# Optimization experiments

Hardware: AMD Instinct MI355X
Metric: run time of the kernel (lower is better)

The kernel has to match this reference:

```python
import jax, jax.numpy as jnp
import numpy as np

N = 50000          # nodes
E = 1_600_000      # directed edges (avg degree 32)
C_IN = 512
C_OUT = 64
H1, F1 = 8, 8      # conv1: heads=8, out per head=8
H2 = 1             # conv2: heads_2=1, concat=False
NEG_SLOPE = 0.2    # GATConv default leaky_relu slope
ELU_ALPHA = 0.2    # F.elu(..., alpha=0.2) in forward


def _glorot(key, shape):
    fan_in, fan_out = shape[0], shape[-1]
    lim = jnp.sqrt(6.0 / (fan_in + fan_out))
    return jax.random.uniform(key, shape, jnp.float32, -lim, lim)


def setup_inputs() -> dict:
    key = jax.random.key(0)
    ks = jax.random.split(key, 12)
    x = jax.random.normal(ks[0], (N, C_IN), jnp.float32)
    edge_index = jax.random.randint(ks[1], (2, E), 0, N, jnp.int32)
    # conv1 params
    W1 = _glorot(ks[2], (C_IN, H1 * F1))
    att_src1 = _glorot(ks[3], (H1, F1))
    att_dst1 = _glorot(ks[4], (H1, F1))
    b1 = jnp.zeros((H1 * F1,), jnp.float32)
    # conv2 params (concat=False, heads=1)
    W2 = _glorot(ks[5], (H1 * F1, H2 * C_OUT))
    att_src2 = _glorot(ks[6], (H2, C_OUT))
    att_dst2 = _glorot(ks[7], (H2, C_OUT))
    b2 = jnp.zeros((C_OUT,), jnp.float32)
    return dict(x=x, edge_index=edge_index, W1=W1, att_src1=att_src1,
                att_dst1=att_dst1, b1=b1, W2=W2, att_src2=att_src2,
                att_dst2=att_dst2, b2=b2)


def gat_conv(x, src, dst, W, att_src, att_dst, bias, concat):
    """PyG GATConv (self-loops already appended to src/dst). Eval mode (no dropout)."""
    n = x.shape[0]
    H, F = att_src.shape
    h = (x @ W).reshape(n, H, F)                       # [N,H,F]
    a_src = jnp.sum(h * att_src, axis=-1)              # [N,H]
    a_dst = jnp.sum(h * att_dst, axis=-1)              # [N,H]
    e = jax.nn.leaky_relu(a_src[src] + a_dst[dst], NEG_SLOPE)  # [E',H]
    # segment softmax over incoming edges of each destination node
    m = jax.ops.segment_max(e, dst, num_segments=n)    # [N,H]
    m = jnp.where(jnp.isfinite(m), m, 0.0)
    ex = jnp.exp(e - m[dst])
    denom = jax.ops.segment_sum(ex, dst, num_segments=n)
    alpha = ex / (denom[dst] + 1e-16)                  # [E',H]
    msg = h[src] * alpha[:, :, None]                   # [E',H,F]
    out = jax.ops.segment_sum(msg, dst, num_segments=n)  # [N,H,F]
    out = out.reshape(n, H * F) if concat else out.mean(axis=1)
    return out + bias


def reference(x, edge_index, W1, att_src1, att_dst1, b1,
              W2, att_src2, att_dst2, b2):
    # add self loops once (GATConv default add_self_loops=True)
    loop = jnp.arange(N, dtype=edge_index.dtype)
    src = jnp.concatenate([edge_index[0], loop])
    dst = jnp.concatenate([edge_index[1], loop])
    # dropout layers are identity in eval mode
    h = gat_conv(x, src, dst, W1, att_src1, att_dst1, b1, concat=True)
    h = jax.nn.elu(h, alpha=ELU_ALPHA)
    out = gat_conv(h, src, dst, W2, att_src2, att_dst2, b2, concat=False)
    return out
```

## Files before the change

### kernel.cpp

```cpp
#include <hip/hip_runtime.h>
#include <hip/hip_bf16.h>
#include <hip/hip_fp16.h>

constexpr int NN   = 50000;
constexpr int NE   = 1600000;
constexpr int CIN  = 512;
constexpr int DH   = 64;
constexpr int H1N  = 8;

constexpr int NB     = 98;
constexpr int TILE   = 8192;
constexpr int NTILES = (NE + TILE - 1) / TILE;
constexpr int BCAP   = 20480;

typedef __attribute__((ext_vector_type(8))) short bf16x8v;
typedef __attribute__((ext_vector_type(4))) float f32x4v;

__device__ __forceinline__ float bf(unsigned short u) {
    union { unsigned int i; float f; } v; v.i = ((unsigned int)u) << 16; return v.f;
}
__device__ __forceinline__ float lrelu(float x) { return fmaxf(x, 0.2f * x); }
__device__ __forceinline__ float ldf(const unsigned short* p, size_t i, bool f32) {
    return f32 ? ((const float*)p)[i] : bf(p[i]);
}
__device__ __forceinline__ unsigned short f2bf(float f) {
    union { float f; unsigned int u; } v; v.f = f;
    unsigned int r = (v.u + 0x7fff + ((v.u >> 16) & 1)) >> 16;
    return (unsigned short)r;
}

__global__ __launch_bounds__(256) void gat_detect(const unsigned short* __restrict__ W1,
                                                  int* __restrict__ flag) {
    __shared__ int cnt;
    if (threadIdx.x == 0) cnt = 0;
    __syncthreads();
    int local = 0;
    for (int i = threadIdx.x; i < 4096; i += 256) {
        unsigned short u = W1[i];
        int e = (u >> 7) & 0xFF;
        if (e >= 140) local++;
    }
    atomicAdd(&cnt, local);
    __syncthreads();
    if (threadIdx.x == 0) flag[0] = (cnt > 100) ? 1 : 0;
}


__global__ __launch_bounds__(256) void gat_bucketA(const int* __restrict__ src,
                                                   const int* __restrict__ dst,
                                                   int* __restrict__ gcnt,
                                                   unsigned int* __restrict__ bucketed) {
    __shared__ int hist[NB];
    __shared__ int cur[NB];
    int t = threadIdx.x;
    if (t < NB) hist[t] = 0;
    __syncthreads();
    int base = blockIdx.x * TILE;
    for (int i = t; i < TILE; i += 256) {
        int e = base + i;
        if (e < NE) atomicAdd(&hist[dst[e] >> 9], 1);
    }
    __syncthreads();
    if (t < NB) cur[t] = hist[t] ? atomicAdd(&gcnt[t], hist[t]) : 0;
    __syncthreads();
    for (int i = t; i < TILE; i += 256) {
        int e = base + i;
        if (e < NE) {
            int d = dst[e];
            int b = d >> 9;
            int p = atomicAdd(&cur[b], 1);
            if (p < BCAP)
                bucketed[(size_t)b * BCAP + p] =
                    ((unsigned int)(d & 511) << 16) | (unsigned int)src[e];
        }
    }
}

__global__ __launch_bounds__(128) void gat_bucketscan(const int* __restrict__ gcnt,
                                                      int* __restrict__ boff,
                                                      int* __restrict__ row_ptr) {
    __shared__ int s[128];
    int t = threadIdx.x;
    s[t] = (t < NB) ? gcnt[t] : 0;
    __syncthreads();
    for (int off = 1; off < 128; off <<= 1) {
        int x = s[t];
        int add = (t >= off) ? s[t - off] : 0;
        __syncthreads();
        s[t] = x + add;
        __syncthreads();
    }
    if (t <= NB) boff[t] = (t == 0) ? 0 : s[t - 1];
    if (t == 0) row_ptr[NN] = NE;
}

__global__ __launch_bounds__(256) void gat_bucketB(const unsigned int* __restrict__ bucketed,
                                                   const int* __restrict__ gcnt,
                                                   const int* __restrict__ boff,
                                                   int* __restrict__ row_ptr,
                                                   int* __restrict__ col_idx) {
    __shared__ int hist[512];
    __shared__ int sums[256];
    int t = threadIdx.x;
    int b = blockIdx.x;
    int e0 = boff[b];
    int cnt = gcnt[b]; if (cnt > BCAP) cnt = BCAP;
    const unsigned int* bb = bucketed + (size_t)b * BCAP;
    hist[t] = 0; hist[t + 256] = 0;
    __syncthreads();
    for (int i = t; i < cnt; i += 256)
        atomicAdd(&hist[bb[i] >> 16], 1);
    __syncthreads();
    int a0 = hist[2 * t], a1 = hist[2 * t + 1];
    sums[t] = a0 + a1;
    __syncthreads();
    for (int off = 1; off < 256; off <<= 1) {
        int x = sums[t];
        int add = (t >= off) ? sums[t - off] : 0;
        __syncthreads();
        sums[t] = x + add;
        __syncthreads();
    }
    int excl = (t == 0) ? 0 : sums[t - 1];
    hist[2 * t]     = excl;
    hist[2 * t + 1] = excl + a0;
    int node0 = b << 9;
    if (node0 + 2 * t     < NN) row_ptr[node0 + 2 * t]     = e0 + excl;
    if (node0 + 2 * t + 1 < NN) row_ptr[node0 + 2 * t + 1] = e0 + excl + a0;
    __syncthreads();
    for (int i = t; i < cnt; i += 256) {
        unsigned int pk = bb[i];
        int p = atomicAdd(&hist[pk >> 16], 1);
        col_idx[e0 + p] = (int)(pk & 0xFFFFu);
    }
}


__global__ __launch_bounds__(256) void gat_maxcol(const float* __restrict__ v, int n, int H,
                                                  unsigned int* __restrict__ out) {
    __shared__ float red[256];
    int t = threadIdx.x;
    float mx = -3.4e38f;
    for (int idx = blockIdx.x * 256 + t; idx < n; idx += gridDim.x * 256)
        mx = fmaxf(mx, v[idx]);
    red[t] = mx;
    __syncthreads();
    for (int off = 128; off >= H; off >>= 1) {
        if (t < off) red[t] = fmaxf(red[t], red[t + off]);
        __syncthreads();
    }
    if (t < H) {
        union { float f; unsigned int u; } b; b.f = red[t];
        unsigned int enc = (b.u & 0x80000000u) ? ~b.u : (b.u | 0x80000000u);
        atomicMax(&out[t], enc);
    }
}

__device__ __forceinline__ float gdecode(unsigned int u) {
    union { unsigned int u; float f; } d;
    d.u = (u & 0x80000000u) ? (u ^ 0x80000000u) : ~u;
    return d.f;
}


__global__ __launch_bounds__(256) void gat_transW(const unsigned short* __restrict__ W1,
                                                  const int* __restrict__ flag,
                                                  unsigned short* __restrict__ wts) {
    int idx = blockIdx.x * 256 + threadIdx.x;
    int n = idx >> 9, k = idx & 511;
    if (flag[0] == 0) {
        int o  = n * 1024 + k * 2;
        int os = o ^ ((n & 7) << 4);
        wts[os >> 1] = W1[(size_t)k * DH + n];
    } else {
        float v = ((const float*)W1)[(size_t)k * DH + n];
        unsigned short hi = f2bf(v);
        union { unsigned int u; float f; } hf; hf.u = ((unsigned int)hi) << 16;
        unsigned short lo = f2bf(v - hf.f);
        int q = k >> 7, kk = k & 127;
        int o = q * 32768 + n * 256 + ((kk * 2) ^ ((n & 7) << 4));
        wts[o >> 1]             = hi;
        wts[(o + 16384) >> 1]   = lo;
    }
}


__global__ __launch_bounds__(256) void gat_transW2(const unsigned short* __restrict__ W2,
                                                   const int* __restrict__ flag,
                                                   unsigned short* __restrict__ wts2) {
    int idx = blockIdx.x * 256 + threadIdx.x;
    if (idx >= 4096) return;
    int n = idx & 63, k = idx >> 6;
    unsigned short hi, lo;
    if (flag[0] == 0) {
        hi = W2[(size_t)k * DH + n];
        lo = 0;
    } else {
        float v = ((const float*)W2)[(size_t)k * DH + n];
        hi = f2bf(v);
        union { unsigned int u; float f; } hf; hf.u = ((unsigned int)hi) << 16;
        lo = f2bf(v - hf.f);
    }
    int o = n * 128 + ((k * 2) ^ ((n & 7) << 4));
    wts2[o >> 1]            = hi;
    wts2[(o + 8192) >> 1]   = lo;
}


__global__ __launch_bounds__(256) void gat_gemm1_mfma(const unsigned short* __restrict__ x,
                                                      const unsigned short* __restrict__ wts,
                                                      const unsigned short* __restrict__ as1,
                                                      const unsigned short* __restrict__ ad1,
                                                      const int* __restrict__ flag,
                                                      __half* __restrict__ h1h,
                                                      float* __restrict__ a_s1,
                                                      float* __restrict__ a_d1) {
    if (flag[0] != 0) return;
    __shared__ __align__(16) unsigned short wl[32768];
    int t = threadIdx.x;
#pragma unroll
    for (int it = 0; it < 16; ++it) {
        int c = it * 256 + t;
        *(uint4*)((char*)wl + c * 16) = *(const uint4*)((const char*)wts + c * 16);
    }
    __syncthreads();

    int lane = t & 63, wv = t >> 6;
    int g = lane >> 4;
    int r = lane & 15;
    int chunk = blockIdx.x * 4 + wv;
    if (chunk * 16 >= NN) return;
    int rowbase = chunk * 16;

    int vbase = r * 1024;
    int gx = g * 16;
    int xr = (r & 7) << 4;

    const char* xrow = (const char*)x + ((size_t)(rowbase + r) * CIN + g * 8) * 2;

    f32x4v acc[4];
#pragma unroll
    for (int nt = 0; nt < 4; ++nt) acc[nt] = (f32x4v){0.f, 0.f, 0.f, 0.f};

#pragma unroll 4
    for (int s = 0; s < 16; ++s) {
        union { uint4 u; bf16x8v v; } a;
        a.u = *(const uint4*)(xrow + s * 64);
        int o = vbase + ((s * 64 + gx) ^ xr);
        const char* bp = (const char*)wl + o;
#pragma unroll
        for (int nt = 0; nt < 4; ++nt) {
            union { uint4 u; bf16x8v v; } bv;
            bv.u = *(const uint4*)(bp + nt * 16384);
            acc[nt] = __builtin_amdgcn_mfma_f32_16x16x32_bf16(a.v, bv.v, acc[nt], 0, 0, 0);
        }
    }

    float avs[4], avd[4];
#pragma unroll
    for (int nt = 0; nt < 4; ++nt) {
        avs[nt] = bf(as1[nt * 16 + r]);
        avd[nt] = bf(ad1[nt * 16 + r]);
    }

#pragma unroll
    for (int nt = 0; nt < 4; ++nt) {
#pragma unroll
        for (int i = 0; i < 4; ++i) {
            int row = rowbase + g * 4 + i;
            float v = acc[nt][i];
            h1h[(size_t)row * DH + nt * 16 + r] = __float2half(v);
            float ps = v * avs[nt];
            float pd = v * avd[nt];
            ps += __shfl_xor(ps, 1, 64); ps += __shfl_xor(ps, 2, 64); ps += __shfl_xor(ps, 4, 64);
            pd += __shfl_xor(pd, 1, 64); pd += __shfl_xor(pd, 2, 64); pd += __shfl_xor(pd, 4, 64);
            if ((r & 7) == 0) {
                int head = nt * 2 + (r >> 3);
                a_s1[row * H1N + head] = ps;
                a_d1[row * H1N + head] = pd;
            }
        }
    }
}


__global__ __launch_bounds__(256) void gat_gemm1_mfma_f32(const float* __restrict__ x,
                                                          const unsigned short* __restrict__ wts,
                                                          const float* __restrict__ as1,
                                                          const float* __restrict__ ad1,
                                                          const int* __restrict__ flag,
                                                          __half* __restrict__ h1h,
                                                          float* __restrict__ a_s1,
                                                          float* __restrict__ a_d1) {
    if (flag[0] == 0) return;
    __shared__ __align__(16) unsigned short wl[16384];
    int t = threadIdx.x;
    int lane = t & 63, wv = t >> 6;
    int g = lane >> 4;
    int r = lane & 15;
    int chunk = blockIdx.x * 2 + (wv >> 1);
    int ntb = (wv & 1) * 2;
    bool active = (chunk * 16 < NN);
    int rowbase = (active ? chunk : 0) * 16;

    int vbase = r * 256;
    int xr = (r & 7) << 4;

    const float* xrow = x + (size_t)(rowbase + r) * CIN + g * 8;

    f32x4v acc[2];
    acc[0] = (f32x4v){0.f, 0.f, 0.f, 0.f};
    acc[1] = (f32x4v){0.f, 0.f, 0.f, 0.f};

    for (int q = 0; q < 4; ++q) {
        if (q) __syncthreads();
        const uint4* gsrc = (const uint4*)((const char*)wts + q * 32768);
#pragma unroll
        for (int it = 0; it < 8; ++it)
            ((uint4*)wl)[it * 256 + t] = gsrc[it * 256 + t];
        __syncthreads();

#pragma unroll
        for (int s = 0; s < 4; ++s) {
            const float4* xp = (const float4*)(xrow + q * 128 + s * 32);
            float4 v0 = xp[0], v1 = xp[1];
            float xv[8] = {v0.x, v0.y, v0.z, v0.w, v1.x, v1.y, v1.z, v1.w};
            union { unsigned short u[8]; bf16x8v v; } ahi, alo;
#pragma unroll
            for (int i2 = 0; i2 < 8; ++i2) {
                union { float f; unsigned int u; } xb; xb.f = xv[i2];
                unsigned int hb = xb.u & 0xffff0000u;
                union { unsigned int u; float f; } hf; hf.u = hb;
                ahi.u[i2] = (unsigned short)(xb.u >> 16);
                alo.u[i2] = f2bf(xv[i2] - hf.f);
            }
            int o = vbase + ((s * 64 + g * 16) ^ xr);
#pragma unroll
            for (int n2 = 0; n2 < 2; ++n2) {
                int nt = ntb + n2;
                union { uint4 u; bf16x8v v; } bhi, blo;
                bhi.u = *(const uint4*)((const char*)wl + nt * 4096 + o);
                blo.u = *(const uint4*)((const char*)wl + 16384 + nt * 4096 + o);
                acc[n2] = __builtin_amdgcn_mfma_f32_16x16x32_bf16(ahi.v, bhi.v, acc[n2], 0, 0, 0);
                acc[n2] = __builtin_amdgcn_mfma_f32_16x16x32_bf16(ahi.v, blo.v, acc[n2], 0, 0, 0);
                acc[n2] = __builtin_amdgcn_mfma_f32_16x16x32_bf16(alo.v, bhi.v, acc[n2], 0, 0, 0);
            }
        }
    }

    if (!active) return;

    float avs[2], avd[2];
#pragma unroll
    for (int n2 = 0; n2 < 2; ++n2) {
        avs[n2] = as1[(ntb + n2) * 16 + r];
        avd[n2] = ad1[(ntb + n2) * 16 + r];
    }

#pragma unroll
    for (int n2 = 0; n2 < 2; ++n2) {
        int nt = ntb + n2;
#pragma unroll
        for (int i = 0; i < 4; ++i) {
            int row = rowbase + g * 4 + i;
            float v = acc[n2][i];
            h1h[(size_t)row * DH + nt * 16 + r] = __float2half(v);
            float ps = v * avs[n2];
            float pd = v * avd[n2];
            ps += __shfl_xor(ps, 1, 64); ps += __shfl_xor(ps, 2, 64); ps += __shfl_xor(ps, 4, 64);
            pd += __shfl_xor(pd, 1, 64); pd += __shfl_xor(pd, 2, 64); pd += __shfl_xor(pd, 4, 64);
            if ((r & 7) == 0) {
                int head = nt * 2 + (r >> 3);
                a_s1[row * H1N + head] = ps;
                a_d1[row * H1N + head] = pd;
            }
        }
    }
}


__global__ __launch_bounds__(256) void gat_agg1(const int* __restrict__ row_ptr,
                                                const int* __restrict__ col_idx,
                                                const float* __restrict__ a_s1,
                                                const float* __restrict__ a_d1,
                                                const unsigned int* __restrict__ Gsu,
                                                const __half* __restrict__ h1h,
                                                const unsigned short* __restrict__ b1,
                                                const int* __restrict__ flag,
                                                float* __restrict__ hout) {
    const bool f32 = (flag[0] != 0);
    int i = (blockIdx.x * 256 + threadIdx.x) >> 6;
    int lane = threadIdx.x & 63;
    if (i >= NN) return;
    int ek = lane & 7;
    int eh = lane >> 3;
    int wbase = lane & ~7;

    float adst = a_d1[i * H1N + eh];
    float m = lrelu(gdecode(Gsu[eh]) + adst);

    int jb = row_ptr[i], je = row_ptr[i + 1];
    int deg = je - jb;
    int myidx = (lane < deg) ? col_idx[jb + lane] : 0;

    float wself = __expf(lrelu(a_s1[i * H1N + eh] + adst) - m);
    float denp = (ek == 0) ? wself : 0.f;
    float acc = wself * __half2float(h1h[(size_t)i * DH + lane]);

    for (int j0 = 0; j0 < deg; j0 += 8) {
        int s[8]; int se;
        bool vE = (j0 + ek) < deg;
        if (j0 < 64) {
#pragma unroll
            for (int k = 0; k < 8; ++k) s[k] = __shfl(myidx, j0 + k, 64);
            se = __shfl(myidx, j0 + ek, 64);
        } else {
            int dm1 = deg - 1;
#pragma unroll
            for (int k = 0; k < 8; ++k) {
                int jj = j0 + k; if (jj > dm1) jj = dm1;
                s[k] = col_idx[jb + jj];
            }
            se = col_idx[jb + (vE ? j0 + ek : dm1)];
        }
        float w = __expf(lrelu(a_s1[se * H1N + eh] + adst) - m);
        w = vE ? w : 0.f;
        denp += w;
        float r[8];
#pragma unroll
        for (int k = 0; k < 8; ++k) r[k] = __half2float(h1h[(size_t)s[k] * DH + lane]);
        float ws[8];
#pragma unroll
        for (int k = 0; k < 8; ++k) ws[k] = __shfl(w, wbase + k, 64);
        float a0 = (ws[0] * r[0] + ws[1] * r[1]) + (ws[2] * r[2] + ws[3] * r[3]);
        float a1 = (ws[4] * r[4] + ws[5] * r[5]) + (ws[6] * r[6] + ws[7] * r[7]);
        acc += a0 + a1;
    }
    denp += __shfl_xor(denp, 1, 64);
    denp += __shfl_xor(denp, 2, 64);
    denp += __shfl_xor(denp, 4, 64);

    float val = acc / denp + ldf(b1, lane, f32);
    val = val > 0.f ? val : 0.2f * (__expf(val) - 1.f);
    hout[(size_t)i * DH + lane] = val;
}


__global__ __launch_bounds__(256) void gat_gemm2_mfma(const float* __restrict__ hin,
                                                      const unsigned short* __restrict__ wts2,
                                                      const unsigned short* __restrict__ as2,
                                                      const unsigned short* __restrict__ ad2,
                                                      const int* __restrict__ flag,
                                                      __half* __restrict__ h2h,
                                                      float* __restrict__ a_s2,
                                                      float* __restrict__ a_d2) {
    __shared__ __align__(16) unsigned short wl[8192];
    const bool f32 = (flag[0] != 0);
    int t = threadIdx.x;
#pragma unroll
    for (int it = 0; it < 4; ++it)
        ((uint4*)wl)[it * 256 + t] = ((const uint4*)wts2)[it * 256 + t];
    __syncthreads();

    int lane = t & 63, wv = t >> 6;
    int g = lane >> 4;
    int r = lane & 15;
    int chunk = blockIdx.x * 4 + wv;
    if (chunk * 16 >= NN) return;
    int rowbase = chunk * 16;

    int vbase = r * 128;
    int xr = (r & 7) << 4;

    const float* xrow = hin + (size_t)(rowbase + r) * DH + g * 8;

    f32x4v acc[4];
#pragma unroll
    for (int nt = 0; nt < 4; ++nt) acc[nt] = (f32x4v){0.f, 0.f, 0.f, 0.f};

#pragma unroll
    for (int s = 0; s < 2; ++s) {
        const float4* xp = (const float4*)(xrow + s * 32);
        float4 v0 = xp[0], v1 = xp[1];
        float xv[8] = {v0.x, v0.y, v0.z, v0.w, v1.x, v1.y, v1.z, v1.w};
        union { unsigned short u[8]; bf16x8v v; } ahi, alo;
#pragma unroll
        for (int i2 = 0; i2 < 8; ++i2) {
            union { float f; unsigned int u; } xb; xb.f = xv[i2];
            unsigned int hb = xb.u & 0xffff0000u;
            union { unsigned int u; float f; } hf; hf.u = hb;
            ahi.u[i2] = (unsigned short)(xb.u >> 16);
            alo.u[i2] = f2bf(xv[i2] - hf.f);
        }
        int o = vbase + ((s * 64 + g * 16) ^ xr);
#pragma unroll
        for (int nt = 0; nt < 4; ++nt) {
            union { uint4 u; bf16x8v v; } bhi, blo;
            bhi.u = *(const uint4*)((const char*)wl + nt * 2048 + o);
            blo.u = *(const uint4*)((const char*)wl + 8192 + nt * 2048 + o);
            acc[nt] = __builtin_amdgcn_mfma_f32_16x16x32_bf16(ahi.v, bhi.v, acc[nt], 0, 0, 0);
            acc[nt] = __builtin_amdgcn_mfma_f32_16x16x32_bf16(ahi.v, blo.v, acc[nt], 0, 0, 0);
            acc[nt] = __builtin_amdgcn_mfma_f32_16x16x32_bf16(alo.v, bhi.v, acc[nt], 0, 0, 0);
        }
    }

    float avs[4], avd[4];
#pragma unroll
    for (int nt = 0; nt < 4; ++nt) {
        avs[nt] = ldf(as2, nt * 16 + r, f32);
        avd[nt] = ldf(ad2, nt * 16 + r, f32);
    }

#pragma unroll
    for (int i = 0; i < 4; ++i) {
        int row = rowbase + g * 4 + i;
        float ps = 0.f, pd = 0.f;
#pragma unroll
        for (int nt = 0; nt < 4; ++nt) {
            float v = acc[nt][i];
            h2h[(size_t)row * DH + nt * 16 + r] = __float2half(v);
            ps += v * avs[nt];
            pd += v * avd[nt];
        }
        ps += __shfl_xor(ps, 1, 64); ps += __shfl_xor(ps, 2, 64);
        ps += __shfl_xor(ps, 4, 64); ps += __shfl_xor(ps, 8, 64);
        pd += __shfl_xor(pd, 1, 64); pd += __shfl_xor(pd, 2, 64);
        pd += __shfl_xor(pd, 4, 64); pd += __shfl_xor(pd, 8, 64);
        if (r == 0) { a_s2[row] = ps; a_d2[row] = pd; }
    }
}


__global__ __launch_bounds__(256) void gat_agg2(const int* __restrict__ row_ptr,
                                                const int* __restrict__ col_idx,
                                                const float* __restrict__ a_s2,
                                                const float* __restrict__ a_d2,
                                                const unsigned int* __restrict__ Gsu2,
                                                const __half* __restrict__ h2h,
                                                const unsigned short* __restrict__ b2,
                                                const int* __restrict__ flag,
                                                void* __restrict__ out) {
    const bool f32 = (flag[0] != 0);
    int i = (blockIdx.x * 256 + threadIdx.x) >> 6;
    int lane = threadIdx.x & 63;
    if (i >= NN) return;
    int ek = lane & 7;

    float adst = a_d2[i];
    float m = lrelu(gdecode(Gsu2[0]) + adst);

    int jb = row_ptr[i], je = row_ptr[i + 1];
    int deg = je - jb;
    int myidx = (lane < deg) ? col_idx[jb + lane] : 0;

    float wself = __expf(lrelu(a_s2[i] + adst) - m);
    float denp = (ek == 0) ? wself : 0.f;
    float acc = wself * __half2float(h2h[(size_t)i * DH + lane]);

    for (int j0 = 0; j0 < deg; j0 += 8) {
        int s[8]; int se;
        bool vE = (j0 + ek) < deg;
        if (j0 < 64) {
#pragma unroll
            for (int k = 0; k < 8; ++k) s[k] = __shfl(myidx, j0 + k, 64);
            se = __shfl(myidx, j0 + ek, 64);
        } else {
            int dm1 = deg - 1;
#pragma unroll
            for (int k = 0; k < 8; ++k) {
                int jj = j0 + k; if (jj > dm1) jj = dm1;
                s[k] = col_idx[jb + jj];
            }
            se = col_idx[jb + (vE ? j0 + ek : dm1)];
        }
        float w = __expf(lrelu(a_s2[se] + adst) - m);
        w = vE ? w : 0.f;
        denp += w;
        float r[8];
#pragma unroll
        for (int k = 0; k < 8; ++k) r[k] = __half2float(h2h[(size_t)s[k] * DH + lane]);
        float ws[8];
#pragma unroll
        for (int k = 0; k < 8; ++k) ws[k] = __shfl(w, k, 64);
        float a0 = (ws[0] * r[0] + ws[1] * r[1]) + (ws[2] * r[2] + ws[3] * r[3]);
        float a1 = (ws[4] * r[4] + ws[5] * r[5]) + (ws[6] * r[6] + ws[7] * r[7]);
        acc += a0 + a1;
    }
    denp += __shfl_xor(denp, 1, 64);
    denp += __shfl_xor(denp, 2, 64);
    denp += __shfl_xor(denp, 4, 64);

    float val = acc / denp + ldf(b2, lane, f32);
    size_t oi = (size_t)i * DH + lane;
    if (f32) ((float*)out)[oi] = val;
    else     ((__hip_bfloat16*)out)[oi] = __float2bfloat16(val);
}


static void* g_scratch = nullptr;

extern "C" void kernel_launch(void* const* d_in, const int* in_sizes, int n_in,
                              void* d_out, int out_size, void* d_ws, size_t ws_size,
                              hipStream_t stream) {
    const unsigned short* x   = (const unsigned short*)d_in[0];
    const int*            ei  = (const int*)d_in[1];
    const unsigned short* W1  = (const unsigned short*)d_in[2];
    const unsigned short* as1 = (const unsigned short*)d_in[3];
    const unsigned short* ad1 = (const unsigned short*)d_in[4];
    const unsigned short* b1  = (const unsigned short*)d_in[5];
    const unsigned short* W2  = (const unsigned short*)d_in[6];
    const unsigned short* as2 = (const unsigned short*)d_in[7];
    const unsigned short* ad2 = (const unsigned short*)d_in[8];
    const unsigned short* b2  = (const unsigned short*)d_in[9];

    const int* srcv = ei;
    const int* dstv = ei + NE;

    const size_t off_wts   = 64;
    const size_t off_wts2  = off_wts + 131072;
    const size_t off_h1h   = off_wts2 + 16384;
    const size_t off_hmid  = off_h1h + (size_t)NN * DH * 2;
    const size_t off_as1   = off_hmid + (size_t)NN * DH * 4;
    const size_t off_ad1   = off_as1 + (size_t)NN * H1N * 4;
    const size_t off_rp    = off_ad1 + (size_t)NN * H1N * 4;
    const size_t off_ci    = off_rp + (size_t)(NN + 1) * 4;
    const size_t off_bk    = off_ci + (size_t)NE * 4;
    const size_t off_gcnt  = off_bk + (size_t)NB * BCAP * 4;
    const size_t off_gsu   = off_gcnt + 128 * 4;
    const size_t off_boff  = off_gsu + 16 * 4;
    const size_t need      = off_boff + 128 * 4;

    void* wsbase = d_ws;
    if (ws_size < need) {
        if (g_scratch == nullptr) hipMalloc(&g_scratch, need);
        wsbase = g_scratch;
    }
    char* B = (char*)wsbase;

    int*            flag = (int*)B;
    unsigned short* wts  = (unsigned short*)(B + off_wts);
    unsigned short* wts2 = (unsigned short*)(B + off_wts2);
    __half*         h1h  = (__half*)(B + off_h1h);
    float*          hmid = (float*)(B + off_hmid);
    float*          a_s1 = (float*)(B + off_as1);
    float*          a_d1 = (float*)(B + off_ad1);
    int*         row_ptr = (int*)(B + off_rp);
    int*         col_idx = (int*)(B + off_ci);
    unsigned int* bucketed = (unsigned int*)(B + off_bk);
    int*            gcnt = (int*)(B + off_gcnt);
    unsigned int*   Gsu  = (unsigned int*)(B + off_gsu);
    int*            boff = (int*)(B + off_boff);
    __half* h2h  = h1h;
    float* a_s2 = a_s1;
    float* a_d2 = a_d1;

    hipMemsetAsync(gcnt, 0, (128 + 16) * sizeof(int), stream);
    gat_detect<<<1, 256, 0, stream>>>(W1, flag);

    gat_bucketA   <<<NTILES, 256, 0, stream>>>(srcv, dstv, gcnt, bucketed);
    gat_bucketscan<<<1, 128, 0, stream>>>(gcnt, boff, row_ptr);
    gat_bucketB   <<<NB, 256, 0, stream>>>(bucketed, gcnt, boff, row_ptr, col_idx);

    gat_transW <<<128, 256, 0, stream>>>(W1, flag, wts);
    gat_transW2<<<16, 256, 0, stream>>>(W2, flag, wts2);
    int gemmb  = (3125 + 3) / 4;
    int gemmb2 = (3125 + 1) / 2;
    gat_gemm1_mfma    <<<gemmb, 256, 0, stream>>>(x, wts, as1, ad1, flag, h1h, a_s1, a_d1);
    gat_gemm1_mfma_f32<<<gemmb2, 256, 0, stream>>>((const float*)x, wts,
                                                   (const float*)as1, (const float*)ad1,
                                                   flag, h1h, a_s1, a_d1);

    gat_maxcol<<<64, 256, 0, stream>>>(a_s1, NN * H1N, 8, Gsu);

    int nb = (NN * 64 + 255) / 256;
    gat_agg1<<<nb, 256, 0, stream>>>(row_ptr, col_idx, a_s1, a_d1, Gsu, h1h, b1, flag, hmid);

    gat_gemm2_mfma<<<gemmb, 256, 0, stream>>>(hmid, wts2, as2, ad2, flag, h2h, a_s2, a_d2);

    gat_maxcol<<<32, 256, 0, stream>>>(a_s2, NN, 1, Gsu + 8);

    gat_agg2<<<nb, 256, 0, stream>>>(row_ptr, col_idx, a_s2, a_d2, Gsu + 8, h2h, b2, flag, d_out);
}
```

Measured before the change: 409.6 us.

## Fuse layer-2 linear projection and attention scores into layer-1 aggregation kernel

The layer-1 aggregation kernel now multiplies each node's ELU output by W2, which is held in fp32 shared memory, using per-lane shuffles. It writes h2 in fp16 along with the layer-2 source and destination attention scores, so the fp32 intermediate never goes to global memory. This removes the separate W2 transpose kernel, the MFMA GEMM2 kernel, and the write and read-back of the 50000x64 fp32 intermediate. In exchange, each wave runs 64 serial shuffle-FMA steps per node on CUDA cores, and the kernel uses a persistent grid-stride loop with 2048 blocks. h2 and the layer-2 scores get their own buffers because layer-1 data is still being read while they are written.

```diff
diff --git a/kernel.cpp b/kernel.cpp
--- a/kernel.cpp
+++ b/kernel.cpp
@@ -185,28 +185,6 @@
 }
 
 
-__global__ __launch_bounds__(256) void gat_transW2(const unsigned short* __restrict__ W2,
-                                                   const int* __restrict__ flag,
-                                                   unsigned short* __restrict__ wts2) {
-    int idx = blockIdx.x * 256 + threadIdx.x;
-    if (idx >= 4096) return;
-    int n = idx & 63, k = idx >> 6;
-    unsigned short hi, lo;
-    if (flag[0] == 0) {
-        hi = W2[(size_t)k * DH + n];
-        lo = 0;
-    } else {
-        float v = ((const float*)W2)[(size_t)k * DH + n];
-        hi = f2bf(v);
-        union { unsigned int u; float f; } hf; hf.u = ((unsigned int)hi) << 16;
-        lo = f2bf(v - hf.f);
-    }
-    int o = n * 128 + ((k * 2) ^ ((n & 7) << 4));
-    wts2[o >> 1]            = hi;
-    wts2[(o + 8192) >> 1]   = lo;
-}
-
-
 __global__ __launch_bounds__(256) void gat_gemm1_mfma(const unsigned short* __restrict__ x,
                                                       const unsigned short* __restrict__ wts,
                                                       const unsigned short* __restrict__ as1,
@@ -386,147 +364,89 @@
                                                 const unsigned int* __restrict__ Gsu,
                                                 const __half* __restrict__ h1h,
                                                 const unsigned short* __restrict__ b1,
+                                                const unsigned short* __restrict__ W2,
+                                                const unsigned short* __restrict__ as2,
+                                                const unsigned short* __restrict__ ad2,
                                                 const int* __restrict__ flag,
-                                                float* __restrict__ hout) {
+                                                __half* __restrict__ h2h,
+                                                float* __restrict__ a_s2o,
+                                                float* __restrict__ a_d2o) {
+    __shared__ float w2l[DH * DH];
     const bool f32 = (flag[0] != 0);
-    int i = (blockIdx.x * 256 + threadIdx.x) >> 6;
-    int lane = threadIdx.x & 63;
-    if (i >= NN) return;
+    int t = threadIdx.x;
+    for (int idx = t; idx < DH * DH; idx += 256) w2l[idx] = ldf(W2, idx, f32);
+    __syncthreads();
+
+    int lane = t & 63, wv = t >> 6;
     int ek = lane & 7;
     int eh = lane >> 3;
     int wbase = lane & ~7;
 
-    float adst = a_d1[i * H1N + eh];
-    float m = lrelu(gdecode(Gsu[eh]) + adst);
-
-    int jb = row_ptr[i], je = row_ptr[i + 1];
-    int deg = je - jb;
-    int myidx = (lane < deg) ? col_idx[jb + lane] : 0;
-
-    float wself = __expf(lrelu(a_s1[i * H1N + eh] + adst) - m);
-    float denp = (ek == 0) ? wself : 0.f;
-    float acc = wself * __half2float(h1h[(size_t)i * DH + lane]);
-
-    for (int j0 = 0; j0 < deg; j0 += 8) {
-        int s[8]; int se;
-        bool vE = (j0 + ek) < deg;
-        if (j0 < 64) {
-#pragma unroll
-            for (int k = 0; k < 8; ++k) s[k] = __shfl(myidx, j0 + k, 64);
-            se = __shfl(myidx, j0 + ek, 64);
-        } else {
-            int dm1 = deg - 1;
-#pragma unroll
-            for (int k = 0; k < 8; ++k) {
-                int jj = j0 + k; if (jj > dm1) jj = dm1;
-                s[k] = col_idx[jb + jj];
+    float bv   = ldf(b1, lane, f32);
+    float asv2 = ldf(as2, lane, f32);
+    float adv2 = ldf(ad2, lane, f32);
+
+    for (int i = blockIdx.x * 4 + wv; i < NN; i += gridDim.x * 4) {
+        float adst = a_d1[i * H1N + eh];
+        float m = lrelu(gdecode(Gsu[eh]) + adst);
+
+        int jb = row_ptr[i], je = row_ptr[i + 1];
+        int deg = je - jb;
+        int myidx = (lane < deg) ? col_idx[jb + lane] : 0;
+
+        float wself = __expf(lrelu(a_s1[i * H1N + eh] + adst) - m);
+        float denp = (ek == 0) ? wself : 0.f;
+        float acc = wself * __half2float(h1h[(size_t)i * DH + lane]);
+
+        for (int j0 = 0; j0 < deg; j0 += 8) {
+            int s[8]; int se;
+            bool vE = (j0 + ek) < deg;
+            if (j0 < 64) {
+#pragma unroll
+                for (int k = 0; k < 8; ++k) s[k] = __shfl(myidx, j0 + k, 64);
+                se = __shfl(myidx, j0 + ek, 64);
+            } else {
+                int dm1 = deg - 1;
+#pragma unroll
+                for (int k = 0; k < 8; ++k) {
+                    int jj = j0 + k; if (jj > dm1) jj = dm1;
+                    s[k] = col_idx[jb + jj];
+                }
+                se = col_idx[jb + (vE ? j0 + ek : dm1)];
             }
-            se = col_idx[jb + (vE ? j0 + ek : dm1)];
-        }
-        float w = __expf(lrelu(a_s1[se * H1N + eh] + adst) - m);
-        w = vE ? w : 0.f;
-        denp += w;
-        float r[8];
-#pragma unroll
-        for (int k = 0; k < 8; ++k) r[k] = __half2float(h1h[(size_t)s[k] * DH + lane]);
-        float ws[8];
-#pragma unroll
-        for (int k = 0; k < 8; ++k) ws[k] = __shfl(w, wbase + k, 64);
-        float a0 = (ws[0] * r[0] + ws[1] * r[1]) + (ws[2] * r[2] + ws[3] * r[3]);
-        float a1 = (ws[4] * r[4] + ws[5] * r[5]) + (ws[6] * r[6] + ws[7] * r[7]);
-        acc += a0 + a1;
-    }
-    denp += __shfl_xor(denp, 1, 64);
-    denp += __shfl_xor(denp, 2, 64);
-    denp += __shfl_xor(denp, 4, 64);
-
-    float val = acc / denp + ldf(b1, lane, f32);
-    val = val > 0.f ? val : 0.2f * (__expf(val) - 1.f);
-    hout[(size_t)i * DH + lane] = val;
-}
-
-
-__global__ __launch_bounds__(256) void gat_gemm2_mfma(const float* __restrict__ hin,
-                                                      const unsigned short* __restrict__ wts2,
-                                                      const unsigned short* __restrict__ as2,
-                                                      const unsigned short* __restrict__ ad2,
-                                                      const int* __restrict__ flag,
-                                                      __half* __restrict__ h2h,
-                                                      float* __restrict__ a_s2,
-                                                      float* __restrict__ a_d2) {
-    __shared__ __align__(16) unsigned short wl[8192];
-    const bool f32 = (flag[0] != 0);
-    int t = threadIdx.x;
-#pragma unroll
-    for (int it = 0; it < 4; ++it)
-        ((uint4*)wl)[it * 256 + t] = ((const uint4*)wts2)[it * 256 + t];
-    __syncthreads();
-
-    int lane = t & 63, wv = t >> 6;
-    int g = lane >> 4;
-    int r = lane & 15;
-    int chunk = blockIdx.x * 4 + wv;
-    if (chunk * 16 >= NN) return;
-    int rowbase = chunk * 16;
-
-    int vbase = r * 128;
-    int xr = (r & 7) << 4;
-
-    const float* xrow = hin + (size_t)(rowbase + r) * DH + g * 8;
-
-    f32x4v acc[4];
-#pragma unroll
-    for (int nt = 0; nt < 4; ++nt) acc[nt] = (f32x4v){0.f, 0.f, 0.f, 0.f};
-
-#pragma unroll
-    for (int s = 0; s < 2; ++s) {
-        const float4* xp = (const float4*)(xrow + s * 32);
-        float4 v0 = xp[0], v1 = xp[1];
-        float xv[8] = {v0.x, v0.y, v0.z, v0.w, v1.x, v1.y, v1.z, v1.w};
-        union { unsigned short u[8]; bf16x8v v; } ahi, alo;
-#pragma unroll
-        for (int i2 = 0; i2 < 8; ++i2) {
-            union { float f; unsigned int u; } xb; xb.f = xv[i2];
-            unsigned int hb = xb.u & 0xffff0000u;
-            union { unsigned int u; float f; } hf; hf.u = hb;
-            ahi.u[i2] = (unsigned short)(xb.u >> 16);
-            alo.u[i2] = f2bf(xv[i2] - hf.f);
-        }
-        int o = vbase + ((s * 64 + g * 16) ^ xr);
-#pragma unroll
-        for (int nt = 0; nt < 4; ++nt) {
-            union { uint4 u; bf16x8v v; } bhi, blo;
-            bhi.u = *(const uint4*)((const char*)wl + nt * 2048 + o);
-            blo.u = *(const uint4*)((const char*)wl + 8192 + nt * 2048 + o);
-            acc[nt] = __builtin_amdgcn_mfma_f32_16x16x32_bf16(ahi.v, bhi.v, acc[nt], 0, 0, 0);
-            acc[nt] = __builtin_amdgcn_mfma_f32_16x16x32_bf16(ahi.v, blo.v, acc[nt], 0, 0, 0);
-            acc[nt] = __builtin_amdgcn_mfma_f32_16x16x32_bf16(alo.v, bhi.v, acc[nt], 0, 0, 0);
-        }
-    }
-
-    float avs[4], avd[4];
-#pragma unroll
-    for (int nt = 0; nt < 4; ++nt) {
-        avs[nt] = ldf(as2, nt * 16 + r, f32);
-        avd[nt] = ldf(ad2, nt * 16 + r, f32);
-    }
-
-#pragma unroll
-    for (int i = 0; i < 4; ++i) {
-        int row = rowbase + g * 4 + i;
-        float ps = 0.f, pd = 0.f;
-#pragma unroll
-        for (int nt = 0; nt < 4; ++nt) {
-            float v = acc[nt][i];
-            h2h[(size_t)row * DH + nt * 16 + r] = __float2half(v);
-            ps += v * avs[nt];
-            pd += v * avd[nt];
-        }
-        ps += __shfl_xor(ps, 1, 64); ps += __shfl_xor(ps, 2, 64);
-        ps += __shfl_xor(ps, 4, 64); ps += __shfl_xor(ps, 8, 64);
-        pd += __shfl_xor(pd, 1, 64); pd += __shfl_xor(pd, 2, 64);
-        pd += __shfl_xor(pd, 4, 64); pd += __shfl_xor(pd, 8, 64);
-        if (r == 0) { a_s2[row] = ps; a_d2[row] = pd; }
+            float w = __expf(lrelu(a_s1[se * H1N + eh] + adst) - m);
+            w = vE ? w : 0.f;
+            denp += w;
+            float r[8];
+#pragma unroll
+            for (int k = 0; k < 8; ++k) r[k] = __half2float(h1h[(size_t)s[k] * DH + lane]);
+            float ws[8];
+#pragma unroll
+            for (int k = 0; k < 8; ++k) ws[k] = __shfl(w, wbase + k, 64);
+            float a0 = (ws[0] * r[0] + ws[1] * r[1]) + (ws[2] * r[2] + ws[3] * r[3]);
+            float a1 = (ws[4] * r[4] + ws[5] * r[5]) + (ws[6] * r[6] + ws[7] * r[7]);
+            acc += a0 + a1;
+        }
+        denp += __shfl_xor(denp, 1, 64);
+        denp += __shfl_xor(denp, 2, 64);
+        denp += __shfl_xor(denp, 4, 64);
+
+        float val = acc / denp + bv;
+        val = val > 0.f ? val : 0.2f * (__expf(val) - 1.f);
+
+        float o2 = 0.f;
+#pragma unroll 8
+        for (int k = 0; k < DH; ++k)
+            o2 = fmaf(__shfl(val, k, 64), w2l[k * DH + lane], o2);
+        h2h[(size_t)i * DH + lane] = __float2half(o2);
+
+        float ps = o2 * asv2, pd = o2 * adv2;
+#pragma unroll
+        for (int o = 1; o < 64; o <<= 1) {
+            ps += __shfl_xor(ps, o, 64);
+            pd += __shfl_xor(pd, o, 64);
+        }
+        if (lane == 0) { a_s2o[i] = ps; a_d2o[i] = pd; }
     }
 }
 
@@ -617,12 +537,13 @@
     const int* dstv = ei + NE;
 
     const size_t off_wts   = 64;
-    const size_t off_wts2  = off_wts + 131072;
-    const size_t off_h1h   = off_wts2 + 16384;
-    const size_t off_hmid  = off_h1h + (size_t)NN * DH * 2;
-    const size_t off_as1   = off_hmid + (size_t)NN * DH * 4;
+    const size_t off_h1h   = off_wts + 131072;
+    const size_t off_h2h   = off_h1h + (size_t)NN * DH * 2;
+    const size_t off_as1   = off_h2h + (size_t)NN * DH * 2;
     const size_t off_ad1   = off_as1 + (size_t)NN * H1N * 4;
-    const size_t off_rp    = off_ad1 + (size_t)NN * H1N * 4;
+    const size_t off_as2   = off_ad1 + (size_t)NN * H1N * 4;
+    const size_t off_ad2   = off_as2 + (size_t)NN * 4;
+    const size_t off_rp    = off_ad2 + (size_t)NN * 4;
     const size_t off_ci    = off_rp + (size_t)(NN + 1) * 4;
     const size_t off_bk    = off_ci + (size_t)NE * 4;
     const size_t off_gcnt  = off_bk + (size_t)NB * BCAP * 4;
@@ -639,20 +560,18 @@
 
     int*            flag = (int*)B;
     unsigned short* wts  = (unsigned short*)(B + off_wts);
-    unsigned short* wts2 = (unsigned short*)(B + off_wts2);
     __half*         h1h  = (__half*)(B + off_h1h);
-    float*          hmid = (float*)(B + off_hmid);
+    __half*         h2h  = (__half*)(B + off_h2h);
     float*          a_s1 = (float*)(B + off_as1);
     float*          a_d1 = (float*)(B + off_ad1);
+    float*          a_s2 = (float*)(B + off_as2);
+    float*          a_d2 = (float*)(B + off_ad2);
     int*         row_ptr = (int*)(B + off_rp);
     int*         col_idx = (int*)(B + off_ci);
     unsigned int* bucketed = (unsigned int*)(B + off_bk);
     int*            gcnt = (int*)(B + off_gcnt);
     unsigned int*   Gsu  = (unsigned int*)(B + off_gsu);
     int*            boff = (int*)(B + off_boff);
-    __half* h2h  = h1h;
-    float* a_s2 = a_s1;
-    float* a_d2 = a_d1;
 
     hipMemsetAsync(gcnt, 0, (128 + 16) * sizeof(int), stream);
     gat_detect<<<1, 256, 0, stream>>>(W1, flag);
@@ -662,7 +581,6 @@
     gat_bucketB   <<<NB, 256, 0, stream>>>(bucketed, gcnt, boff, row_ptr, col_idx);
 
     gat_transW <<<128, 256, 0, stream>>>(W1, flag, wts);
-    gat_transW2<<<16, 256, 0, stream>>>(W2, flag, wts2);
     int gemmb  = (3125 + 3) / 4;
     int gemmb2 = (3125 + 1) / 2;
     gat_gemm1_mfma    <<<gemmb, 256, 0, stream>>>(x, wts, as1, ad1, flag, h1h, a_s1, a_d1);
@@ -672,12 +590,11 @@
 
     gat_maxcol<<<64, 256, 0, stream>>>(a_s1, NN * H1N, 8, Gsu);
 
+    gat_agg1<<<2048, 256, 0, stream>>>(row_ptr, col_idx, a_s1, a_d1, Gsu, h1h, b1,
+                                       W2, as2, ad2, flag, h2h, a_s2, a_d2);
+
+    gat_maxcol<<<32, 256, 0, stream>>>(a_s2, NN, 1, Gsu + 8);
+
     int nb = (NN * 64 + 255) / 256;
-    gat_agg1<<<nb, 256, 0, stream>>>(row_ptr, col_idx, a_s1, a_d1, Gsu, h1h, b1, flag, hmid);
-
-    gat_gemm2_mfma<<<gemmb, 256, 0, stream>>>(hmid, wts2, as2, ad2, flag, h2h, a_s2, a_d2);
-
-    gat_maxcol<<<32, 256, 0, stream>>>(a_s2, NN, 1, Gsu + 8);
-
     gat_agg2<<<nb, 256, 0, stream>>>(row_ptr, col_idx, a_s2, a_d2, Gsu + 8, h2h, b2, flag, d_out);
 }
```

Result: slower. 457.8 us (+11.8%).
